# Kernel tuning notes

Hardware: AMD Instinct MI355X
Metric: run time of the kernel (lower is better)

Reference implementation:

```python
import jax, jax.numpy as jnp
import numpy as np

N = 40000      # nodes
E = 640000     # edges
IN_DIM = 128
HID = 128
HEADS = 4
DHEAD = HID // HEADS  # 32
LAYERS = 3
TIMESTEPS = 2
NEG_SLOPE = 0.2


def setup_inputs() -> dict:
    key = jax.random.key(0)
    ks = jax.random.split(key, 16)
    s = 0.05
    inp = {
        "node_feats": jax.random.normal(ks[0], (N, IN_DIM), jnp.float32),
        "src": jax.random.randint(ks[1], (E,), 0, N, jnp.int32),
        "dst": jax.random.randint(ks[2], (E,), 0, N, jnp.int32),
        "proj_W": jax.random.normal(ks[3], (IN_DIM, HID), jnp.float32) * s,
        "proj_b": jnp.zeros((HID,), jnp.float32),
        "fc_W": jax.random.normal(ks[4], (LAYERS, HID, HID), jnp.float32) * s,
        "attn_l": jax.random.normal(ks[5], (LAYERS, HEADS, DHEAD), jnp.float32) * s,
        "attn_r": jax.random.normal(ks[6], (LAYERS, HEADS, DHEAD), jnp.float32) * s,
        "conv_bias": jnp.zeros((LAYERS, HID), jnp.float32),
        "gru_Wih": jax.random.normal(ks[7], (3 * HID, HID), jnp.float32) * s,
        "gru_Whh": jax.random.normal(ks[8], (3 * HID, HID), jnp.float32) * s,
        "gru_bih": jnp.zeros((3 * HID,), jnp.float32),
        "gru_bhh": jnp.zeros((3 * HID,), jnp.float32),
    }
    return inp


def _gat_layer(h, src, dst, fc_W, attn_l, attn_r, bias):
    # h: (N, HID). DGL GATConv: fc -> edge attn -> segment softmax -> scatter sum
    feat = (h @ fc_W).reshape(N, HEADS, DHEAD)
    el = jnp.einsum('nhd,hd->nh', feat, attn_l)  # (N, H)
    er = jnp.einsum('nhd,hd->nh', feat, attn_r)
    e = jax.nn.leaky_relu(el[src] + er[dst], NEG_SLOPE)  # (E, H)
    # segment softmax over incoming edges per destination node
    emax = jax.ops.segment_max(e, dst, num_segments=N)  # (N, H)
    ee = jnp.exp(e - emax[dst])
    denom = jax.ops.segment_sum(ee, dst, num_segments=N)
    alpha = ee / denom[dst]  # (E, H)
    msg = feat[src] * alpha[:, :, None]  # (E, H, D)
    rst = jax.ops.segment_sum(msg, dst, num_segments=N)  # (N, H, D)
    rst = rst + h.reshape(N, HEADS, DHEAD)          # identity residual
    rst = rst + bias.reshape(HEADS, DHEAD)          # learned bias
    return jax.nn.elu(rst).reshape(N, HID)


def _gru_step(x, Wih, Whh, bih, bhh):
    # seq_len == 1, h0 == 0 -> recurrent matmul Whh @ h0 vanishes; b_hh remains
    gi = x @ Wih.T + bih  # (N, 3*HID)
    r = jax.nn.sigmoid(gi[:, :HID] + bhh[:HID])
    z = jax.nn.sigmoid(gi[:, HID:2 * HID] + bhh[HID:2 * HID])
    n = jnp.tanh(gi[:, 2 * HID:] + r * bhh[2 * HID:])
    return (1.0 - z) * n


def reference(node_feats, src, dst, proj_W, proj_b, fc_W, attn_l, attn_r,
              conv_bias, gru_Wih, gru_Whh, gru_bih, gru_bhh):
    h = node_feats @ proj_W + proj_b
    for l in range(LAYERS):
        h = _gat_layer(h, src, dst, fc_W[l], attn_l[l], attn_r[l], conv_bias[l])
    for _ in range(TIMESTEPS):
        h = _gru_step(h, gru_Wih, gru_Whh, gru_bih, gru_bhh)
    return h
```

## Files before the change

kernel.cpp:

```cpp
#include <hip/hip_runtime.h>
#include <hip/hip_bf16.h>

#define NNODES 40000
#define NEDGES 640000
#define M2PAD  40064
#define HID    128
#define WSTRIDE (NEDGES + 16)

typedef __attribute__((ext_vector_type(8))) short bf16x8;
typedef __attribute__((ext_vector_type(4))) float f32x4;

__device__ __forceinline__ float bl(unsigned u){ return __uint_as_float(u << 16); }
__device__ __forceinline__ float bh(unsigned u){ return __uint_as_float(u & 0xFFFF0000u); }
__device__ __forceinline__ unsigned short f2b(float f){
    unsigned u = __float_as_uint(f);
    u = (u + 0x7FFFu + ((u >> 16) & 1u)) >> 16;
    return (unsigned short)u;
}
__device__ __forceinline__ float fast_rcp(float x){ return __builtin_amdgcn_rcpf(x); }

__device__ __forceinline__ void g2l16(const void* g, void* l){
    __builtin_amdgcn_global_load_lds(
        (const __attribute__((address_space(1))) unsigned int*)g,
        (__attribute__((address_space(3))) unsigned int*)l, 16, 0, 0);
}

__global__ void prep_all(const float* __restrict__ node_feats,
                         const float* __restrict__ proj_W, const float* __restrict__ fc_W,
                         const float* __restrict__ gru_Wih,
                         unsigned short* __restrict__ nf,
                         unsigned short* __restrict__ projWT, unsigned short* __restrict__ fcWT,
                         unsigned short* __restrict__ gruWb){
    int b = blockIdx.x;
    if (b < 5000){
        int gid = b * 256 + threadIdx.x;
        float4 v = ((const float4*)node_feats)[gid];
        ushort4 o;
        o.x = f2b(v.x); o.y = f2b(v.y); o.z = f2b(v.z); o.w = f2b(v.w);
        ((ushort4*)nf)[gid] = o;
    } else if (b < 5256){
        int t = b - 5000;
        int c = t >> 6;
        int idx = (t & 63) * 256 + threadIdx.x;
        const float* in   = (c == 0) ? proj_W : fc_W + (size_t)(c - 1) * 16384;
        unsigned short* o = (c == 0) ? projWT : fcWT + (size_t)(c - 1) * 16384;
        int k = idx >> 7, n = idx & 127;
        o[n * 128 + k] = f2b(in[idx]);
    } else {
        int idx = (b - 5256) * 256 + threadIdx.x;
        gruWb[idx] = f2b(gru_Wih[idx]);
    }
}

__global__ void count_kernel(const int* __restrict__ dst, int* __restrict__ deg){
    int e = blockIdx.x * 256 + threadIdx.x;
    atomicAdd(&deg[dst[e]], 1);
}

__global__ __launch_bounds__(1024) void scan_kernel(const int* __restrict__ deg,
        int* __restrict__ rowptr, int* __restrict__ cur, int Nn){
    __shared__ int wsum[17];
    __shared__ int carry;
    int t = threadIdx.x, lane = t & 63, wid = t >> 6;
    if (t == 0) carry = 0;
    __syncthreads();
    for (int base = 0; base < Nn; base += 1024){
        int idx = base + t;
        int v = (idx < Nn) ? deg[idx] : 0;
        int x = v;
        #pragma unroll
        for (int d = 1; d < 64; d <<= 1){
            int y = __shfl_up(x, d, 64);
            if (lane >= d) x += y;
        }
        if (lane == 63) wsum[wid] = x;
        __syncthreads();
        if (wid == 0){
            int vv = (lane < 16) ? wsum[lane] : 0;
            int xx = vv;
            #pragma unroll
            for (int d = 1; d < 16; d <<= 1){
                int y = __shfl_up(xx, d, 64);
                if (lane >= d) xx += y;
            }
            if (lane < 16) wsum[lane] = xx - vv;
            if (lane == 15) wsum[16] = xx;
        }
        __syncthreads();
        int excl = carry + wsum[wid] + (x - v);
        if (idx < Nn){ rowptr[idx] = excl; cur[idx] = excl; }
        __syncthreads();
        if (t == 0) carry += wsum[16];
        __syncthreads();
    }
    if (threadIdx.x == 0) rowptr[Nn] = carry;
}

__global__ void fill_kernel(const int* __restrict__ src, const int* __restrict__ dst,
                            int* __restrict__ cur, int* __restrict__ esrc,
                            int* __restrict__ edst){
    int e = blockIdx.x * 256 + threadIdx.x;
    int d = dst[e];
    int pos = atomicAdd(&cur[d], 1);
    esrc[pos] = src[e];
    edst[pos] = d;
}

template<int MT>
__global__ __launch_bounds__(256) void gemm_t(
        const unsigned short* __restrict__ A, const unsigned short* __restrict__ BT,
        const float* __restrict__ bias, void* __restrict__ C,
        int Mreal, int ldc, int outF32,
        const float* __restrict__ al, const float* __restrict__ ar,
        float* __restrict__ elp, float* __restrict__ erp)
{
    __shared__ unsigned char lds[MT * 256 + 32768];
    unsigned char* ldsA = lds;
    unsigned char* ldsB = lds + MT * 256;
    int w = threadIdx.x >> 6, lane = threadIdx.x & 63;
    int rsub = lane >> 4, c16 = lane & 15;
    long baseM = (long)blockIdx.x * MT;
    long baseN = (long)blockIdx.y * 128;

    #pragma unroll
    for (int i = 0; i < MT / 16; i++){
        int chunk = w * (MT / 16) + i;
        int r = chunk * 4 + rsub;
        int cg = c16 ^ (r & 15);
        long ar_ = baseM + r; if (ar_ >= Mreal) ar_ = Mreal - 1;
        g2l16((const unsigned char*)A + ar_ * 256 + cg * 16, ldsA + chunk * 1024);
    }
    #pragma unroll
    for (int i = 0; i < 8; i++){
        int chunk = w * 8 + i;
        int r = chunk * 4 + rsub;
        int cg = c16 ^ (r & 15);
        long br = baseN + r;
        g2l16((const unsigned char*)BT + br * 256 + cg * 16, ldsB + chunk * 1024);
    }
    __syncthreads();

    constexpr int MI = 4;
    constexpr int NI = (MT == 128) ? 4 : 2;
    int mo = (MT == 128) ? (w & 1) * 64 : 0;
    int no = (MT == 128) ? (w >> 1) * 64 : w * 32;
    int q = lane >> 4, cl = lane & 15;
    f32x4 acc[MI][NI];
    #pragma unroll
    for (int i = 0; i < MI; i++)
        #pragma unroll
        for (int j = 0; j < NI; j++) acc[i][j] = (f32x4){0.f, 0.f, 0.f, 0.f};

    #pragma unroll
    for (int kc = 0; kc < 4; kc++){
        bf16x8 av[MI], bv[NI];
        #pragma unroll
        for (int mi = 0; mi < MI; mi++){
            int row = mo + mi * 16 + cl;
            int cs = (kc * 4 + q) ^ (row & 15);
            av[mi] = *(const bf16x8*)(ldsA + row * 256 + cs * 16);
        }
        #pragma unroll
        for (int ni = 0; ni < NI; ni++){
            int row = no + ni * 16 + cl;
            int cs = (kc * 4 + q) ^ (row & 15);
            bv[ni] = *(const bf16x8*)(ldsB + row * 256 + cs * 16);
        }
        #pragma unroll
        for (int mi = 0; mi < MI; mi++)
            #pragma unroll
            for (int ni = 0; ni < NI; ni++)
                acc[mi][ni] = __builtin_amdgcn_mfma_f32_16x16x32_bf16(av[mi], bv[ni], acc[mi][ni], 0, 0, 0);
    }

    #pragma unroll
    for (int mi = 0; mi < MI; mi++){
        #pragma unroll
        for (int ni = 0; ni < NI; ni++){
            int gn = (int)baseN + no + ni * 16 + cl;
            float bvf = bias ? bias[gn] : 0.f;
            long gm0 = baseM + mo + mi * 16 + q * 4;
            #pragma unroll
            for (int reg = 0; reg < 4; reg++){
                float v = acc[mi][ni][reg] + bvf;
                long gm = gm0 + reg;
                if (gm < Mreal){
                    if (outF32) ((float*)C)[gm * ldc + gn] = v;
                    else ((unsigned short*)C)[gm * ldc + gn] = f2b(v);
                }
            }
        }
    }

    if (NI == 2 && al){
        float al_lo = al[no + cl], al_hi = al[no + 16 + cl];
        float ar_lo = ar[no + cl], ar_hi = ar[no + 16 + cl];
        #pragma unroll
        for (int mi = 0; mi < MI; mi++){
            #pragma unroll
            for (int reg = 0; reg < 4; reg++){
                float pl = acc[mi][0][reg] * al_lo + acc[mi][1][reg] * al_hi;
                float pr = acc[mi][0][reg] * ar_lo + acc[mi][1][reg] * ar_hi;
                #pragma unroll
                for (int msk = 8; msk; msk >>= 1){
                    pl += __shfl_xor(pl, msk, 64);
                    pr += __shfl_xor(pr, msk, 64);
                }
                long gm = baseM + mi * 16 + q * 4 + reg;
                if (cl == 0 && gm < Mreal){
                    elp[gm * 4 + w] = pl;
                    erp[gm * 4 + w] = pr;
                }
            }
        }
    }
}

__global__ __launch_bounds__(256) void gru_fused(
        const unsigned short* __restrict__ A, const unsigned short* __restrict__ BT,
        const float* __restrict__ bih, const float* __restrict__ bhh,
        void* __restrict__ out, int Mreal, int outF32)
{
    __shared__ unsigned char ldsA[16384];
    __shared__ unsigned char ldsB[32768];
    int w = threadIdx.x >> 6, lane = threadIdx.x & 63;
    int rsub = lane >> 4, c16 = lane & 15;
    long baseM = (long)blockIdx.x * 64;

    #pragma unroll
    for (int i = 0; i < 4; i++){
        int chunk = w * 4 + i;
        int r = chunk * 4 + rsub;
        int cg = c16 ^ (r & 15);
        long ar = baseM + r; if (ar >= Mreal) ar = Mreal - 1;
        g2l16((const unsigned char*)A + ar * 256 + cg * 16, ldsA + chunk * 1024);
    }

    int no = w * 32;
    int q = lane >> 4, cl = lane & 15;
    f32x4 acc[3][4][2];
    #pragma unroll
    for (int c = 0; c < 3; c++)
        #pragma unroll
        for (int i = 0; i < 4; i++)
            #pragma unroll
            for (int j = 0; j < 2; j++) acc[c][i][j] = (f32x4){0.f, 0.f, 0.f, 0.f};

    for (int c = 0; c < 3; c++){
        if (c) __syncthreads();
        #pragma unroll
        for (int i = 0; i < 8; i++){
            int chunk = w * 8 + i;
            int r = chunk * 4 + rsub;
            int cg = c16 ^ (r & 15);
            long br = c * 128 + r;
            g2l16((const unsigned char*)BT + br * 256 + cg * 16, ldsB + chunk * 1024);
        }
        __syncthreads();
        #pragma unroll
        for (int kc = 0; kc < 4; kc++){
            bf16x8 av[4], bv[2];
            #pragma unroll
            for (int mi = 0; mi < 4; mi++){
                int row = mi * 16 + cl;
                int cs = (kc * 4 + q) ^ (row & 15);
                av[mi] = *(const bf16x8*)(ldsA + row * 256 + cs * 16);
            }
            #pragma unroll
            for (int ni = 0; ni < 2; ni++){
                int row = no + ni * 16 + cl;
                int cs = (kc * 4 + q) ^ (row & 15);
                bv[ni] = *(const bf16x8*)(ldsB + row * 256 + cs * 16);
            }
            #pragma unroll
            for (int mi = 0; mi < 4; mi++)
                #pragma unroll
                for (int ni = 0; ni < 2; ni++)
                    acc[c][mi][ni] = __builtin_amdgcn_mfma_f32_16x16x32_bf16(av[mi], bv[ni], acc[c][mi][ni], 0, 0, 0);
        }
    }

    #pragma unroll
    for (int ni = 0; ni < 2; ni++){
        int j = no + ni * 16 + cl;
        float bir = bih[j]       + bhh[j];
        float biz = bih[128 + j] + bhh[128 + j];
        float bin = bih[256 + j];
        float bhn = bhh[256 + j];
        #pragma unroll
        for (int mi = 0; mi < 4; mi++){
            long gm0 = baseM + mi * 16 + q * 4;
            #pragma unroll
            for (int reg = 0; reg < 4; reg++){
                long n_row = gm0 + reg;
                float gr = acc[0][mi][ni][reg] + bir;
                float gz = acc[1][mi][ni][reg] + biz;
                float gn = acc[2][mi][ni][reg] + bin;
                float r = fast_rcp(1.f + __expf(-gr));
                float z = fast_rcp(1.f + __expf(-gz));
                float ex = __expf(2.f * (gn + r * bhn));
                float nn = (ex - 1.f) * fast_rcp(ex + 1.f);
                float v = (1.f - z) * nn;
                if (n_row < Mreal){
                    if (outF32) ((float*)out)[n_row * 128 + j] = v;
                    else ((unsigned short*)out)[n_row * 128 + j] = f2b(v);
                }
            }
        }
    }
}

__global__ void edge_w(const int* __restrict__ esrc, const int* __restrict__ edst,
                       const float* __restrict__ el, const float* __restrict__ er,
                       float* __restrict__ wgtT){
    int p = blockIdx.x * 256 + threadIdx.x;
    int sn = esrc[p], dn = edst[p];
    float4 l = *(const float4*)(el + (size_t)sn * 4);
    float4 r = *(const float4*)(er + (size_t)dn * 4);
    float e;
    e = l.x + r.x; e = (e > 0.f) ? e : 0.2f * e; wgtT[0 * WSTRIDE + p] = __expf(e);
    e = l.y + r.y; e = (e > 0.f) ? e : 0.2f * e; wgtT[1 * WSTRIDE + p] = __expf(e);
    e = l.z + r.z; e = (e > 0.f) ? e : 0.2f * e; wgtT[2 * WSTRIDE + p] = __expf(e);
    e = l.w + r.w; e = (e > 0.f) ? e : 0.2f * e; wgtT[3 * WSTRIDE + p] = __expf(e);
}

__global__ __launch_bounds__(256) void aggregate(
        const int* __restrict__ rowptr, const int* __restrict__ esrc,
        const float* __restrict__ wgtT,
        const unsigned short* __restrict__ feat, const float* __restrict__ bias,
        unsigned short* __restrict__ h)
{
    int wid = threadIdx.x >> 6, lane = threadIdx.x & 63;
    int n = blockIdx.x * 4 + wid;
    int hh = lane >> 4;
    int d0 = lane * 2;
    int beg = rowptr[n], end = rowptr[n + 1];
    float s = 0.f, a0 = 0.f, a1 = 0.f;
    const unsigned short* fb = feat + d0;
    const float* wplane = wgtT + (size_t)hh * WSTRIDE;

    if (beg < end){
        int p0 = beg & ~7;
        int4 sA = *(const int4*)(esrc + p0);
        int4 sB = *(const int4*)(esrc + p0 + 4);
        float4 wA = make_float4(0.f,0.f,0.f,0.f), wB = wA;
        unsigned f0=0,f1=0,f2=0,f3=0,f4=0,f5=0,f6=0,f7=0;
        int pg = p0 - 8;
        for (int p = p0; p < end; p += 8){
            float4 wcA = *(const float4*)(wplane + p);
            float4 wcB = *(const float4*)(wplane + p + 4);
            unsigned c0 = *(const unsigned*)(fb + (size_t)sA.x * 128);
            unsigned c1 = *(const unsigned*)(fb + (size_t)sA.y * 128);
            unsigned c2 = *(const unsigned*)(fb + (size_t)sA.z * 128);
            unsigned c3 = *(const unsigned*)(fb + (size_t)sA.w * 128);
            unsigned c4 = *(const unsigned*)(fb + (size_t)sB.x * 128);
            unsigned c5 = *(const unsigned*)(fb + (size_t)sB.y * 128);
            unsigned c6 = *(const unsigned*)(fb + (size_t)sB.z * 128);
            unsigned c7 = *(const unsigned*)(fb + (size_t)sB.w * 128);
            int4 nA = *(const int4*)(esrc + p + 8);
            int4 nB = *(const int4*)(esrc + p + 12);
            float w0 = (pg + 0 >= beg && pg + 0 < end) ? wA.x : 0.f;
            float w1 = (pg + 1 >= beg && pg + 1 < end) ? wA.y : 0.f;
            float w2 = (pg + 2 >= beg && pg + 2 < end) ? wA.z : 0.f;
            float w3 = (pg + 3 >= beg && pg + 3 < end) ? wA.w : 0.f;
            float w4 = (pg + 4 >= beg && pg + 4 < end) ? wB.x : 0.f;
            float w5 = (pg + 5 >= beg && pg + 5 < end) ? wB.y : 0.f;
            float w6 = (pg + 6 >= beg && pg + 6 < end) ? wB.z : 0.f;
            float w7 = (pg + 7 >= beg && pg + 7 < end) ? wB.w : 0.f;
            s += ((w0 + w1) + (w2 + w3)) + ((w4 + w5) + (w6 + w7));
            a0 = fmaf(w0, bl(f0), fmaf(w1, bl(f1), fmaf(w2, bl(f2), fmaf(w3, bl(f3), a0))));
            a0 = fmaf(w4, bl(f4), fmaf(w5, bl(f5), fmaf(w6, bl(f6), fmaf(w7, bl(f7), a0))));
            a1 = fmaf(w0, bh(f0), fmaf(w1, bh(f1), fmaf(w2, bh(f2), fmaf(w3, bh(f3), a1))));
            a1 = fmaf(w4, bh(f4), fmaf(w5, bh(f5), fmaf(w6, bh(f6), fmaf(w7, bh(f7), a1))));
            wA = wcA; wB = wcB;
            f0 = c0; f1 = c1; f2 = c2; f3 = c3; f4 = c4; f5 = c5; f6 = c6; f7 = c7;
            sA = nA; sB = nB; pg = p;
        }
        float w0 = (pg + 0 >= beg && pg + 0 < end) ? wA.x : 0.f;
        float w1 = (pg + 1 >= beg && pg + 1 < end) ? wA.y : 0.f;
        float w2 = (pg + 2 >= beg && pg + 2 < end) ? wA.z : 0.f;
        float w3 = (pg + 3 >= beg && pg + 3 < end) ? wA.w : 0.f;
        float w4 = (pg + 4 >= beg && pg + 4 < end) ? wB.x : 0.f;
        float w5 = (pg + 5 >= beg && pg + 5 < end) ? wB.y : 0.f;
        float w6 = (pg + 6 >= beg && pg + 6 < end) ? wB.z : 0.f;
        float w7 = (pg + 7 >= beg && pg + 7 < end) ? wB.w : 0.f;
        s += ((w0 + w1) + (w2 + w3)) + ((w4 + w5) + (w6 + w7));
        a0 = fmaf(w0, bl(f0), fmaf(w1, bl(f1), fmaf(w2, bl(f2), fmaf(w3, bl(f3), a0))));
        a0 = fmaf(w4, bl(f4), fmaf(w5, bl(f5), fmaf(w6, bl(f6), fmaf(w7, bl(f7), a0))));
        a1 = fmaf(w0, bh(f0), fmaf(w1, bh(f1), fmaf(w2, bh(f2), fmaf(w3, bh(f3), a1))));
        a1 = fmaf(w4, bh(f4), fmaf(w5, bh(f5), fmaf(w6, bh(f6), fmaf(w7, bh(f7), a1))));
    }
    float inv = (s > 0.f) ? fast_rcp(s) : 0.f;
    unsigned hv = *(const unsigned*)(h + (size_t)n * 128 + d0);
    float x0 = a0 * inv + bl(hv) + bias[d0];
    float x1 = a1 * inv + bh(hv) + bias[d0 + 1];
    x0 = (x0 > 0.f) ? x0 : expm1f(x0);
    x1 = (x1 > 0.f) ? x1 : expm1f(x1);
    unsigned outv = (unsigned)f2b(x0) | ((unsigned)f2b(x1) << 16);
    *(unsigned*)(h + (size_t)n * 128 + d0) = outv;
}

extern "C" void kernel_launch(void* const* d_in, const int* in_sizes, int n_in,
                              void* d_out, int out_size, void* d_ws, size_t ws_size,
                              hipStream_t stream) {
    const float* node_feats = (const float*)d_in[0];
    const int*   srcp       = (const int*)d_in[1];
    const int*   dstp       = (const int*)d_in[2];
    const float* proj_W     = (const float*)d_in[3];
    const float* proj_b     = (const float*)d_in[4];
    const float* fc_W       = (const float*)d_in[5];
    const float* attn_l     = (const float*)d_in[6];
    const float* attn_r     = (const float*)d_in[7];
    const float* conv_bias  = (const float*)d_in[8];
    const float* gru_Wih    = (const float*)d_in[9];
    const float* gru_bih    = (const float*)d_in[11];
    const float* gru_bhh    = (const float*)d_in[12];
    float* outp = (float*)d_out;

    char* ws = (char*)d_ws;
    size_t off = 0;
    auto carve = [&](size_t bytes) -> char* {
        char* p = ws + off;
        off += (bytes + 255) & ~(size_t)255;
        return p;
    };
    int*            deg    = (int*)carve((size_t)NNODES * 4);
    int*            rowptr = (int*)carve((size_t)(NNODES + 1) * 4);
    int*            cur    = (int*)carve((size_t)NNODES * 4);
    int*            esrc   = (int*)carve((size_t)(NEDGES + 16) * 4);
    int*            edst   = (int*)carve((size_t)NEDGES * 4);
    float*          el     = (float*)carve((size_t)NNODES * 4 * 4);
    float*          er     = (float*)carve((size_t)NNODES * 4 * 4);
    float*          wgtT   = (float*)carve((size_t)4 * WSTRIDE * 4);
    unsigned short* projWT = (unsigned short*)carve(16384 * 2);
    unsigned short* fcWT   = (unsigned short*)carve(3 * 16384 * 2);
    unsigned short* gruWb  = (unsigned short*)carve(49152 * 2);
    unsigned short* nf     = (unsigned short*)carve((size_t)NNODES * 128 * 2);
    unsigned short* h      = (unsigned short*)carve((size_t)M2PAD * 128 * 2);
    unsigned short* feat   = (unsigned short*)carve((size_t)M2PAD * 128 * 2);
    (void)ws_size; (void)in_sizes; (void)n_in; (void)out_size;

    hipMemsetAsync(deg, 0, (size_t)NNODES * 4, stream);
    prep_all<<<5448, 256, 0, stream>>>(node_feats, proj_W, fc_W, gru_Wih, nf, projWT, fcWT, gruWb);
    count_kernel<<<NEDGES / 256, 256, 0, stream>>>(dstp, deg);
    scan_kernel<<<1, 1024, 0, stream>>>(deg, rowptr, cur, NNODES);
    fill_kernel<<<NEDGES / 256, 256, 0, stream>>>(srcp, dstp, cur, esrc, edst);

    gemm_t<64><<<dim3(625, 1), 256, 0, stream>>>(nf, projWT, proj_b, h, NNODES, 128, 0,
                                                 nullptr, nullptr, nullptr, nullptr);

    for (int l = 0; l < 3; l++){
        gemm_t<64><<<dim3(625, 1), 256, 0, stream>>>(h, fcWT + l * 16384, nullptr, feat, NNODES, 128, 0,
                                                     attn_l + l * 128, attn_r + l * 128, el, er);
        edge_w<<<NEDGES / 256, 256, 0, stream>>>(esrc, edst, el, er, wgtT);
        aggregate<<<NNODES / 4, 256, 0, stream>>>(rowptr, esrc, wgtT, feat, conv_bias + l * 128, h);
    }

    gru_fused<<<625, 256, 0, stream>>>(h, gruWb, gru_bih, gru_bhh, h, NNODES, 0);
    gru_fused<<<625, 256, 0, stream>>>(h, gruWb, gru_bih, gru_bhh, outp, NNODES, 1);
}
```

Before: 403.8 us.

## Pad CSR rows to multiples of eight and drop per-edge bounds masking

Each node's in-degree is rounded up to a multiple of 8 in the scan, so every CSR row starts aligned and holds whole groups of 8 edges. Padding slots are filled with src 0 and dst -1, and edge_w writes zero weights for them. The aggregate loop can then drop its per-edge range checks and use 32-bit byte offsets for the gathers. The in-degree count kernel is also folded into prep_all. The cost is more edge slots in edge_w and in the weight arrays, plus two extra memsets.

```diff
diff --git a/kernel.cpp b/kernel.cpp
--- a/kernel.cpp
+++ b/kernel.cpp
@@ -5,7 +5,8 @@
 #define NEDGES 640000
 #define M2PAD  40064
 #define HID    128
-#define WSTRIDE (NEDGES + 16)
+#define PADCAP 920064
+#define WSTRIDE_P (PADCAP + 16)
 
 typedef __attribute__((ext_vector_type(8))) short bf16x8;
 typedef __attribute__((ext_vector_type(4))) float f32x4;
@@ -27,10 +28,10 @@
 
 __global__ void prep_all(const float* __restrict__ node_feats,
                          const float* __restrict__ proj_W, const float* __restrict__ fc_W,
-                         const float* __restrict__ gru_Wih,
+                         const float* __restrict__ gru_Wih, const int* __restrict__ dstp,
                          unsigned short* __restrict__ nf,
                          unsigned short* __restrict__ projWT, unsigned short* __restrict__ fcWT,
-                         unsigned short* __restrict__ gruWb){
+                         unsigned short* __restrict__ gruWb, int* __restrict__ deg){
     int b = blockIdx.x;
     if (b < 5000){
         int gid = b * 256 + threadIdx.x;
@@ -46,15 +47,13 @@
         unsigned short* o = (c == 0) ? projWT : fcWT + (size_t)(c - 1) * 16384;
         int k = idx >> 7, n = idx & 127;
         o[n * 128 + k] = f2b(in[idx]);
-    } else {
+    } else if (b < 5448){
         int idx = (b - 5256) * 256 + threadIdx.x;
         gruWb[idx] = f2b(gru_Wih[idx]);
-    }
-}
-
-__global__ void count_kernel(const int* __restrict__ dst, int* __restrict__ deg){
-    int e = blockIdx.x * 256 + threadIdx.x;
-    atomicAdd(&deg[dst[e]], 1);
+    } else {
+        int e = (b - 5448) * 256 + threadIdx.x;
+        atomicAdd(&deg[dstp[e]], 1);
+    }
 }
 
 __global__ __launch_bounds__(1024) void scan_kernel(const int* __restrict__ deg,
@@ -66,7 +65,7 @@
     __syncthreads();
     for (int base = 0; base < Nn; base += 1024){
         int idx = base + t;
-        int v = (idx < Nn) ? deg[idx] : 0;
+        int v = (idx < Nn) ? ((deg[idx] + 7) & ~7) : 0;
         int x = v;
         #pragma unroll
         for (int d = 1; d < 64; d <<= 1){
@@ -314,14 +313,22 @@
                        const float* __restrict__ el, const float* __restrict__ er,
                        float* __restrict__ wgtT){
     int p = blockIdx.x * 256 + threadIdx.x;
-    int sn = esrc[p], dn = edst[p];
+    int dn = edst[p];
+    if (dn < 0){
+        wgtT[0 * WSTRIDE_P + p] = 0.f;
+        wgtT[1 * WSTRIDE_P + p] = 0.f;
+        wgtT[2 * WSTRIDE_P + p] = 0.f;
+        wgtT[3 * WSTRIDE_P + p] = 0.f;
+        return;
+    }
+    int sn = esrc[p];
     float4 l = *(const float4*)(el + (size_t)sn * 4);
     float4 r = *(const float4*)(er + (size_t)dn * 4);
     float e;
-    e = l.x + r.x; e = (e > 0.f) ? e : 0.2f * e; wgtT[0 * WSTRIDE + p] = __expf(e);
-    e = l.y + r.y; e = (e > 0.f) ? e : 0.2f * e; wgtT[1 * WSTRIDE + p] = __expf(e);
-    e = l.z + r.z; e = (e > 0.f) ? e : 0.2f * e; wgtT[2 * WSTRIDE + p] = __expf(e);
-    e = l.w + r.w; e = (e > 0.f) ? e : 0.2f * e; wgtT[3 * WSTRIDE + p] = __expf(e);
+    e = l.x + r.x; e = (e > 0.f) ? e : 0.2f * e; wgtT[0 * WSTRIDE_P + p] = __expf(e);
+    e = l.y + r.y; e = (e > 0.f) ? e : 0.2f * e; wgtT[1 * WSTRIDE_P + p] = __expf(e);
+    e = l.z + r.z; e = (e > 0.f) ? e : 0.2f * e; wgtT[2 * WSTRIDE_P + p] = __expf(e);
+    e = l.w + r.w; e = (e > 0.f) ? e : 0.2f * e; wgtT[3 * WSTRIDE_P + p] = __expf(e);
 }
 
 __global__ __launch_bounds__(256) void aggregate(
@@ -334,61 +341,46 @@
     int n = blockIdx.x * 4 + wid;
     int hh = lane >> 4;
     int d0 = lane * 2;
+    unsigned doff = (unsigned)(d0 * 2);
     int beg = rowptr[n], end = rowptr[n + 1];
     float s = 0.f, a0 = 0.f, a1 = 0.f;
-    const unsigned short* fb = feat + d0;
-    const float* wplane = wgtT + (size_t)hh * WSTRIDE;
+    const char* fbc = (const char*)feat;
+    const float* wp = wgtT + (size_t)hh * WSTRIDE_P + beg;
+    const int*   ep = esrc + beg;
 
     if (beg < end){
-        int p0 = beg & ~7;
-        int4 sA = *(const int4*)(esrc + p0);
-        int4 sB = *(const int4*)(esrc + p0 + 4);
+        int4 sA = *(const int4*)(ep);
+        int4 sB = *(const int4*)(ep + 4);
         float4 wA = make_float4(0.f,0.f,0.f,0.f), wB = wA;
         unsigned f0=0,f1=0,f2=0,f3=0,f4=0,f5=0,f6=0,f7=0;
-        int pg = p0 - 8;
-        for (int p = p0; p < end; p += 8){
-            float4 wcA = *(const float4*)(wplane + p);
-            float4 wcB = *(const float4*)(wplane + p + 4);
-            unsigned c0 = *(const unsigned*)(fb + (size_t)sA.x * 128);
-            unsigned c1 = *(const unsigned*)(fb + (size_t)sA.y * 128);
-            unsigned c2 = *(const unsigned*)(fb + (size_t)sA.z * 128);
-            unsigned c3 = *(const unsigned*)(fb + (size_t)sA.w * 128);
-            unsigned c4 = *(const unsigned*)(fb + (size_t)sB.x * 128);
-            unsigned c5 = *(const unsigned*)(fb + (size_t)sB.y * 128);
-            unsigned c6 = *(const unsigned*)(fb + (size_t)sB.z * 128);
-            unsigned c7 = *(const unsigned*)(fb + (size_t)sB.w * 128);
-            int4 nA = *(const int4*)(esrc + p + 8);
-            int4 nB = *(const int4*)(esrc + p + 12);
-            float w0 = (pg + 0 >= beg && pg + 0 < end) ? wA.x : 0.f;
-            float w1 = (pg + 1 >= beg && pg + 1 < end) ? wA.y : 0.f;
-            float w2 = (pg + 2 >= beg && pg + 2 < end) ? wA.z : 0.f;
-            float w3 = (pg + 3 >= beg && pg + 3 < end) ? wA.w : 0.f;
-            float w4 = (pg + 4 >= beg && pg + 4 < end) ? wB.x : 0.f;
-            float w5 = (pg + 5 >= beg && pg + 5 < end) ? wB.y : 0.f;
-            float w6 = (pg + 6 >= beg && pg + 6 < end) ? wB.z : 0.f;
-            float w7 = (pg + 7 >= beg && pg + 7 < end) ? wB.w : 0.f;
-            s += ((w0 + w1) + (w2 + w3)) + ((w4 + w5) + (w6 + w7));
-            a0 = fmaf(w0, bl(f0), fmaf(w1, bl(f1), fmaf(w2, bl(f2), fmaf(w3, bl(f3), a0))));
-            a0 = fmaf(w4, bl(f4), fmaf(w5, bl(f5), fmaf(w6, bl(f6), fmaf(w7, bl(f7), a0))));
-            a1 = fmaf(w0, bh(f0), fmaf(w1, bh(f1), fmaf(w2, bh(f2), fmaf(w3, bh(f3), a1))));
-            a1 = fmaf(w4, bh(f4), fmaf(w5, bh(f5), fmaf(w6, bh(f6), fmaf(w7, bh(f7), a1))));
+        for (int p = beg; p < end; p += 8){
+            float4 wcA = *(const float4*)(wp);
+            float4 wcB = *(const float4*)(wp + 4);
+            unsigned c0 = *(const unsigned*)(fbc + ((((unsigned)sA.x) << 8) + doff));
+            unsigned c1 = *(const unsigned*)(fbc + ((((unsigned)sA.y) << 8) + doff));
+            unsigned c2 = *(const unsigned*)(fbc + ((((unsigned)sA.z) << 8) + doff));
+            unsigned c3 = *(const unsigned*)(fbc + ((((unsigned)sA.w) << 8) + doff));
+            unsigned c4 = *(const unsigned*)(fbc + ((((unsigned)sB.x) << 8) + doff));
+            unsigned c5 = *(const unsigned*)(fbc + ((((unsigned)sB.y) << 8) + doff));
+            unsigned c6 = *(const unsigned*)(fbc + ((((unsigned)sB.z) << 8) + doff));
+            unsigned c7 = *(const unsigned*)(fbc + ((((unsigned)sB.w) << 8) + doff));
+            int4 nA = *(const int4*)(ep + 8);
+            int4 nB = *(const int4*)(ep + 12);
+            s += ((wA.x + wA.y) + (wA.z + wA.w)) + ((wB.x + wB.y) + (wB.z + wB.w));
+            a0 = fmaf(wA.x, bl(f0), fmaf(wA.y, bl(f1), fmaf(wA.z, bl(f2), fmaf(wA.w, bl(f3), a0))));
+            a0 = fmaf(wB.x, bl(f4), fmaf(wB.y, bl(f5), fmaf(wB.z, bl(f6), fmaf(wB.w, bl(f7), a0))));
+            a1 = fmaf(wA.x, bh(f0), fmaf(wA.y, bh(f1), fmaf(wA.z, bh(f2), fmaf(wA.w, bh(f3), a1))));
+            a1 = fmaf(wB.x, bh(f4), fmaf(wB.y, bh(f5), fmaf(wB.z, bh(f6), fmaf(wB.w, bh(f7), a1))));
             wA = wcA; wB = wcB;
             f0 = c0; f1 = c1; f2 = c2; f3 = c3; f4 = c4; f5 = c5; f6 = c6; f7 = c7;
-            sA = nA; sB = nB; pg = p;
-        }
-        float w0 = (pg + 0 >= beg && pg + 0 < end) ? wA.x : 0.f;
-        float w1 = (pg + 1 >= beg && pg + 1 < end) ? wA.y : 0.f;
-        float w2 = (pg + 2 >= beg && pg + 2 < end) ? wA.z : 0.f;
-        float w3 = (pg + 3 >= beg && pg + 3 < end) ? wA.w : 0.f;
-        float w4 = (pg + 4 >= beg && pg + 4 < end) ? wB.x : 0.f;
-        float w5 = (pg + 5 >= beg && pg + 5 < end) ? wB.y : 0.f;
-        float w6 = (pg + 6 >= beg && pg + 6 < end) ? wB.z : 0.f;
-        float w7 = (pg + 7 >= beg && pg + 7 < end) ? wB.w : 0.f;
-        s += ((w0 + w1) + (w2 + w3)) + ((w4 + w5) + (w6 + w7));
-        a0 = fmaf(w0, bl(f0), fmaf(w1, bl(f1), fmaf(w2, bl(f2), fmaf(w3, bl(f3), a0))));
-        a0 = fmaf(w4, bl(f4), fmaf(w5, bl(f5), fmaf(w6, bl(f6), fmaf(w7, bl(f7), a0))));
-        a1 = fmaf(w0, bh(f0), fmaf(w1, bh(f1), fmaf(w2, bh(f2), fmaf(w3, bh(f3), a1))));
-        a1 = fmaf(w4, bh(f4), fmaf(w5, bh(f5), fmaf(w6, bh(f6), fmaf(w7, bh(f7), a1))));
+            sA = nA; sB = nB;
+            wp += 8; ep += 8;
+        }
+        s += ((wA.x + wA.y) + (wA.z + wA.w)) + ((wB.x + wB.y) + (wB.z + wB.w));
+        a0 = fmaf(wA.x, bl(f0), fmaf(wA.y, bl(f1), fmaf(wA.z, bl(f2), fmaf(wA.w, bl(f3), a0))));
+        a0 = fmaf(wB.x, bl(f4), fmaf(wB.y, bl(f5), fmaf(wB.z, bl(f6), fmaf(wB.w, bl(f7), a0))));
+        a1 = fmaf(wA.x, bh(f0), fmaf(wA.y, bh(f1), fmaf(wA.z, bh(f2), fmaf(wA.w, bh(f3), a1))));
+        a1 = fmaf(wB.x, bh(f4), fmaf(wB.y, bh(f5), fmaf(wB.z, bh(f6), fmaf(wB.w, bh(f7), a1))));
     }
     float inv = (s > 0.f) ? fast_rcp(s) : 0.f;
     unsigned hv = *(const unsigned*)(h + (size_t)n * 128 + d0);
@@ -427,11 +419,11 @@
     int*            deg    = (int*)carve((size_t)NNODES * 4);
     int*            rowptr = (int*)carve((size_t)(NNODES + 1) * 4);
     int*            cur    = (int*)carve((size_t)NNODES * 4);
-    int*            esrc   = (int*)carve((size_t)(NEDGES + 16) * 4);
-    int*            edst   = (int*)carve((size_t)NEDGES * 4);
+    int*            esrc   = (int*)carve((size_t)(PADCAP + 32) * 4);
+    int*            edst   = (int*)carve((size_t)PADCAP * 4);
     float*          el     = (float*)carve((size_t)NNODES * 4 * 4);
     float*          er     = (float*)carve((size_t)NNODES * 4 * 4);
-    float*          wgtT   = (float*)carve((size_t)4 * WSTRIDE * 4);
+    float*          wgtT   = (float*)carve((size_t)4 * WSTRIDE_P * 4);
     unsigned short* projWT = (unsigned short*)carve(16384 * 2);
     unsigned short* fcWT   = (unsigned short*)carve(3 * 16384 * 2);
     unsigned short* gruWb  = (unsigned short*)carve(49152 * 2);
@@ -441,8 +433,10 @@
     (void)ws_size; (void)in_sizes; (void)n_in; (void)out_size;
 
     hipMemsetAsync(deg, 0, (size_t)NNODES * 4, stream);
-    prep_all<<<5448, 256, 0, stream>>>(node_feats, proj_W, fc_W, gru_Wih, nf, projWT, fcWT, gruWb);
-    count_kernel<<<NEDGES / 256, 256, 0, stream>>>(dstp, deg);
+    hipMemsetAsync(esrc, 0, (size_t)(PADCAP + 32) * 4, stream);
+    hipMemsetAsync(edst, 0xFF, (size_t)PADCAP * 4, stream);
+    prep_all<<<7948, 256, 0, stream>>>(node_feats, proj_W, fc_W, gru_Wih, dstp,
+                                       nf, projWT, fcWT, gruWb, deg);
     scan_kernel<<<1, 1024, 0, stream>>>(deg, rowptr, cur, NNODES);
     fill_kernel<<<NEDGES / 256, 256, 0, stream>>>(srcp, dstp, cur, esrc, edst);
 
@@ -452,7 +446,7 @@
     for (int l = 0; l < 3; l++){
         gemm_t<64><<<dim3(625, 1), 256, 0, stream>>>(h, fcWT + l * 16384, nullptr, feat, NNODES, 128, 0,
                                                      attn_l + l * 128, attn_r + l * 128, el, er);
-        edge_w<<<NEDGES / 256, 256, 0, stream>>>(esrc, edst, el, er, wgtT);
+        edge_w<<<PADCAP / 256, 256, 0, stream>>>(esrc, edst, el, er, wgtT);
         aggregate<<<NNODES / 4, 256, 0, stream>>>(rowptr, esrc, wgtT, feat, conv_bias + l * 128, h);
     }
 
```

Result: no change. 398.1 us (-1.4%).
